# Optimization experiments

Measured on AMD Instinct MI355X. Metric: run time of the kernel, lower is better.

## Reference

```python
import jax, jax.numpy as jnp
import numpy as np

B, S, E, H = 4, 2048, 1024, 16
DK = E // H  # 64


def setup_inputs() -> dict:
    key = jax.random.key(0)
    ks = jax.random.split(key, 6)
    scale = 1.0 / np.sqrt(E)
    return {
        "x": jax.random.normal(ks[0], (B, S, E), dtype=jnp.float32),
        "Wq": jax.random.normal(ks[1], (E, E), dtype=jnp.float32) * scale,
        "Wk": jax.random.normal(ks[2], (E, E), dtype=jnp.float32) * scale,
        "Wv": jax.random.normal(ks[3], (E, E), dtype=jnp.float32) * scale,
        "Wo": jax.random.normal(ks[4], (E, E), dtype=jnp.float32) * scale,
        "theta": jax.random.normal(ks[5], (DK,), dtype=jnp.float32),
    }


def _heads(t):
    # [B,S,E] -> [B,H,S,DK]
    b, s, _ = t.shape
    return t.reshape(b, s, H, DK).transpose(0, 2, 1, 3)


def reference(x, Wq, Wk, Wv, Wo, theta):
    # nn.Linear (no bias): y = x @ W.T
    # quantum transform: independent single-qubit RX(x)->RX(theta)->  <Z> = cos(x+theta)
    q = jnp.cos(_heads(x @ Wq.T) + theta)  # [B,H,S,DK]
    k = jnp.cos(_heads(x @ Wk.T) + theta)
    v = jnp.cos(_heads(x @ Wv.T) + theta)
    scores = jnp.einsum("bhqd,bhkd->bhqk", q, k) / jnp.sqrt(jnp.float32(DK))
    attn = jax.nn.softmax(scores, axis=-1)  # dropout is identity in eval
    out = jnp.einsum("bhqk,bhkd->bhqd", attn, v)  # [B,H,S,DK]
    out = out.transpose(0, 2, 1, 3).reshape(x.shape[0], -1, E)
    return out @ Wo.T
```

## Files before the change

kernel.cpp:

```cpp
#include <hip/hip_runtime.h>

#define B_  4
#define S_  2048
#define E_  1024
#define H_  16
#define DK_ 64
#define M_  (B_*S_)

typedef __attribute__((ext_vector_type(8)))  short short8;
typedef __attribute__((ext_vector_type(4)))  float f32x4;
typedef __attribute__((ext_vector_type(16))) float f32x16;

#define QSCALE 0.18033688f

__device__ __forceinline__ unsigned short f2b(float f) {
    union { float f; unsigned u; } v; v.f = f;
    unsigned u = v.u;
    return (unsigned short)((u + 0x7fffu + ((u >> 16) & 1u)) >> 16);
}

__device__ __forceinline__ void gload_lds16(const unsigned short* g, unsigned short* l) {
    __builtin_amdgcn_global_load_lds((const __attribute__((address_space(1))) void*)g,
                                     (__attribute__((address_space(3))) void*)l, 16, 0, 0);
}

#define XN4 (M_*E_/4)
#define WN4 (E_*E_/4)
__global__ __launch_bounds__(256) void cvt_all(
    const float* __restrict__ x,
    const float* __restrict__ w0, const float* __restrict__ w1,
    const float* __restrict__ w2, const float* __restrict__ w3,
    unsigned short* __restrict__ xb, unsigned short* __restrict__ wb,
    unsigned short* __restrict__ wob) {
    int i = blockIdx.x * 256 + threadIdx.x;
    const float* src;
    unsigned short* dst;
    int idx;
    if (i < XN4) { src = x; dst = xb; idx = i; }
    else {
        int j = i - XN4;
        int z = j >> 18;
        idx = j & (WN4 - 1);
        src = (z == 0) ? w0 : (z == 1) ? w1 : (z == 2) ? w2 : w3;
        dst = (z < 3) ? wb + (size_t)z * E_ * E_ : wob;
    }
    float4 f = ((const float4*)src)[idx];
    ushort4 o;
    o.x = f2b(f.x); o.y = f2b(f.y); o.z = f2b(f.z); o.w = f2b(f.w);
    ((ushort4*)dst)[idx] = o;
}

__global__ __launch_bounds__(256) void gemm_qkv(
    const unsigned short* __restrict__ xb,
    const unsigned short* __restrict__ Wb,
    const float* __restrict__ theta,
    unsigned short* __restrict__ qb,
    unsigned short* __restrict__ kb,
    unsigned short* __restrict__ vtb)
{
    __shared__ unsigned short smem[128*144];
    unsigned short* As = smem;
    unsigned short* Bs = smem + 128*64;
    const int tid = threadIdx.x;
    const int w = tid >> 6, lane = tid & 63, quad = lane >> 4, col = lane & 15;
    const int wm = (w & 1) * 64, wn = (w >> 1) * 64;
    const int m0 = blockIdx.x * 128, n0 = blockIdx.y * 128, z = blockIdx.z;
    const unsigned short* Wz = Wb + (size_t)z * E_ * E_;
    const int srow = lane >> 3, schunk = (lane & 7) * 8;

    f32x4 acc[4][4] = {};
    for (int k0 = 0; k0 < E_; k0 += 64) {
        #pragma unroll
        for (int c = 0; c < 4; c++) {
            int row = w*32 + c*8 + srow;
            gload_lds16(&xb[(size_t)(m0+row)*E_ + k0 + schunk], &As[(w*32 + c*8)*64]);
            gload_lds16(&Wz[(size_t)(n0+row)*E_ + k0 + schunk], &Bs[(w*32 + c*8)*64]);
        }
        __syncthreads();
        #pragma unroll
        for (int kk = 0; kk < 64; kk += 32) {
            short8 a[4], b[4];
            #pragma unroll
            for (int i = 0; i < 4; i++)
                a[i] = *(const short8*)&As[(wm + i*16 + col)*64 + kk + quad*8];
            #pragma unroll
            for (int j = 0; j < 4; j++)
                b[j] = *(const short8*)&Bs[(wn + j*16 + col)*64 + kk + quad*8];
            #pragma unroll
            for (int i = 0; i < 4; i++)
                #pragma unroll
                for (int j = 0; j < 4; j++)
                    acc[i][j] = __builtin_amdgcn_mfma_f32_16x16x32_bf16(a[i], b[j], acc[i][j], 0, 0, 0);
        }
        __syncthreads();
    }

    const int bblk = m0 >> 11;
    const int sbase = m0 & (S_-1);

    if (z != 2) {
        const float qs = (z == 0) ? QSCALE : 1.0f;
        #pragma unroll
        for (int j = 0; j < 4; j++) {
            int nl = wn + j*16 + col;
            float th = theta[(n0 + nl) & 63];
            #pragma unroll
            for (int i = 0; i < 4; i++)
                #pragma unroll
                for (int r = 0; r < 4; r++) {
                    int ml = wm + i*16 + quad*4 + r;
                    int nls = nl ^ (((ml >> 2) & 3) << 4);
                    smem[ml*144 + nls] = f2b(__cosf(acc[i][j][r] + th) * qs);
                }
        }
        __syncthreads();
        unsigned short* dst = (z == 0) ? qb : kb;
        const int h0 = n0 >> 6;
        #pragma unroll
        for (int k = 0; k < 8; k++) {
            int idx = k*256 + tid;
            int chunk = idx & 7, seg = idx >> 3;
            int ml = seg >> 1, hh = seg & 1;
            int ch = chunk ^ (((ml >> 2) & 3) << 1);
            int4 val = *(const int4*)&smem[ml*144 + hh*64 + ch*8];
            size_t g = ((size_t)(bblk*H_ + h0 + hh)*S_ + sbase + ml)*DK_ + chunk*8;
            *(int4*)&dst[g] = val;
        }
    } else {
        #pragma unroll
        for (int j = 0; j < 4; j++) {
            int nl = wn + j*16 + col;
            float th = theta[(n0 + nl) & 63];
            #pragma unroll
            for (int i = 0; i < 4; i++)
                #pragma unroll
                for (int r = 0; r < 4; r++)
                    smem[nl*136 + wm + i*16 + quad*4 + r] = f2b(__cosf(acc[i][j][r] + th));
        }
        __syncthreads();
        int row = tid >> 1, halfm = (tid & 1) * 64;
        int n = n0 + row, h = n >> 6, d = n & 63;
        size_t base = ((size_t)(bblk*H_ + h)*DK_ + d)*S_ + sbase + halfm;
        #pragma unroll
        for (int k = 0; k < 8; k++)
            *(int4*)&vtb[base + k*8] = *(const int4*)&smem[row*136 + halfm + k*8];
    }
}

__global__ __launch_bounds__(256) void gemm_out(
    const unsigned short* __restrict__ ctx,
    const unsigned short* __restrict__ Wob,
    float* __restrict__ out)
{
    __shared__ unsigned short As[128*64];
    __shared__ unsigned short Bs[128*64];
    const int tid = threadIdx.x;
    const int w = tid >> 6, lane = tid & 63, quad = lane >> 4, col = lane & 15;
    const int wm = (w & 1) * 64, wn = (w >> 1) * 64;
    const int m0 = blockIdx.x * 128, n0 = blockIdx.y * 128;
    const int srow = lane >> 3, schunk = (lane & 7) * 8;

    f32x4 acc[4][4] = {};
    for (int k0 = 0; k0 < E_; k0 += 64) {
        #pragma unroll
        for (int c = 0; c < 4; c++) {
            int row = w*32 + c*8 + srow;
            gload_lds16(&ctx[(size_t)(m0+row)*E_ + k0 + schunk], &As[(w*32 + c*8)*64]);
            gload_lds16(&Wob[(size_t)(n0+row)*E_ + k0 + schunk], &Bs[(w*32 + c*8)*64]);
        }
        __syncthreads();
        #pragma unroll
        for (int kk = 0; kk < 64; kk += 32) {
            short8 a[4], b[4];
            #pragma unroll
            for (int i = 0; i < 4; i++)
                a[i] = *(const short8*)&As[(wm + i*16 + col)*64 + kk + quad*8];
            #pragma unroll
            for (int j = 0; j < 4; j++)
                b[j] = *(const short8*)&Bs[(wn + j*16 + col)*64 + kk + quad*8];
            #pragma unroll
            for (int i = 0; i < 4; i++)
                #pragma unroll
                for (int j = 0; j < 4; j++)
                    acc[i][j] = __builtin_amdgcn_mfma_f32_16x16x32_bf16(a[i], b[j], acc[i][j], 0, 0, 0);
        }
        __syncthreads();
    }
    #pragma unroll
    for (int j = 0; j < 4; j++) {
        int n = n0 + wn + j*16 + col;
        #pragma unroll
        for (int i = 0; i < 4; i++)
            #pragma unroll
            for (int r = 0; r < 4; r++) {
                int m = m0 + wm + i*16 + quad*4 + r;
                out[(size_t)m*E_ + n] = acc[i][j][r];
            }
    }
}

#define LPK 72

__global__ __launch_bounds__(256, 2) void flash_attn(
    const unsigned short* __restrict__ qb,
    const unsigned short* __restrict__ kb,
    const unsigned short* __restrict__ vtb,
    unsigned short* __restrict__ ctx)
{
    __shared__ unsigned short Kt[64*LPK];
    __shared__ unsigned short Vt[64*LPK];
    const int tid = threadIdx.x;
    const int w = tid >> 6, lane = tid & 63, col = lane & 31, half = lane >> 5;
    const int q0 = blockIdx.x * 256;
    const int bh = blockIdx.y;

    union U8 { unsigned u[4]; short8 s8; };

    short8 qf[2][4];
    #pragma unroll
    for (int qg = 0; qg < 2; qg++) {
        const unsigned short* qrow = qb + ((size_t)bh*S_ + q0 + w*64 + qg*32 + col)*DK_;
        #pragma unroll
        for (int c = 0; c < 4; c++)
            qf[qg][c] = *(const short8*)&qrow[c*16 + half*8];
    }

    float rsum[2] = {0.f, 0.f};
    f32x16 oacc[2][2] = {};

    for (int kt = 0; kt < S_; kt += 64) {
        __syncthreads();
        for (int i = tid; i < 512; i += 256) {
            int row = i >> 3, c8 = (i & 7) * 8;
            *(int4*)&Kt[row*LPK + c8] = *(const int4*)&kb [((size_t)bh*S_  + kt + row)*DK_ + c8];
            *(int4*)&Vt[row*LPK + c8] = *(const int4*)&vtb[((size_t)bh*DK_ + row)*S_ + kt + c8];
        }
        __syncthreads();

        #pragma unroll
        for (int t = 0; t < 2; t++) {
            short8 kf[4];
            #pragma unroll
            for (int c = 0; c < 4; c++)
                kf[c] = *(const short8*)&Kt[(t*32 + col)*LPK + c*16 + half*8];
            short8 vf[2][2];
            #pragma unroll
            for (int kc = 0; kc < 2; kc++)
                #pragma unroll
                for (int dt = 0; dt < 2; dt++)
                    vf[kc][dt] = *(const short8*)&Vt[(dt*32 + col)*LPK + t*32 + kc*16 + half*8];

            #pragma unroll
            for (int qg = 0; qg < 2; qg++) {
                f32x16 sacc = {};
                #pragma unroll
                for (int c = 0; c < 4; c++)
                    sacc = __builtin_amdgcn_mfma_f32_32x32x16_bf16(kf[c], qf[qg][c], sacc, 0, 0, 0);
                unsigned pk[4][2];
                #pragma unroll
                for (int rg = 0; rg < 4; rg++) {
                    float p0 = __builtin_amdgcn_exp2f(sacc[rg*4+0]);
                    float p1 = __builtin_amdgcn_exp2f(sacc[rg*4+1]);
                    float p2 = __builtin_amdgcn_exp2f(sacc[rg*4+2]);
                    float p3 = __builtin_amdgcn_exp2f(sacc[rg*4+3]);
                    rsum[qg] += (p0 + p1) + (p2 + p3);
                    pk[rg][0] = __builtin_amdgcn_perm(__float_as_uint(p1), __float_as_uint(p0), 0x07060302u);
                    pk[rg][1] = __builtin_amdgcn_perm(__float_as_uint(p3), __float_as_uint(p2), 0x07060302u);
                }
                #pragma unroll
                for (int kc = 0; kc < 2; kc++) {
                    const int lo = 2*kc, hi = 2*kc + 1;
                    unsigned t0 = half ? pk[lo][0] : pk[hi][0];
                    unsigned t1 = half ? pk[lo][1] : pk[hi][1];
                    unsigned r0 = __shfl_xor((int)t0, 32);
                    unsigned r1 = __shfl_xor((int)t1, 32);
                    U8 pa;
                    pa.u[0] = half ? r0 : pk[lo][0];
                    pa.u[1] = half ? r1 : pk[lo][1];
                    pa.u[2] = half ? pk[hi][0] : r0;
                    pa.u[3] = half ? pk[hi][1] : r1;
                    #pragma unroll
                    for (int dt = 0; dt < 2; dt++)
                        oacc[qg][dt] = __builtin_amdgcn_mfma_f32_32x32x16_bf16(pa.s8, vf[kc][dt], oacc[qg][dt], 0, 0, 0);
                }
            }
        }
    }

    const int b = bh >> 4, h = bh & 15;
    #pragma unroll
    for (int qg = 0; qg < 2; qg++) {
        float l = rsum[qg] + __shfl_xor(rsum[qg], 32);
        float inv = 1.0f / l;
        #pragma unroll
        for (int rg = 0; rg < 4; rg++)
            #pragma unroll
            for (int rr = 0; rr < 4; rr++) {
                int row = rr + rg*8 + half*4;
                float invr = __shfl(inv, row);
                int s = q0 + w*64 + qg*32 + row;
                size_t rowoff = ((size_t)(b*S_ + s))*E_ + h*64;
                #pragma unroll
                for (int dt = 0; dt < 2; dt++)
                    ctx[rowoff + dt*32 + col] = f2b(oacc[qg][dt][rg*4 + rr] * invr);
            }
    }
}

extern "C" void kernel_launch(void* const* d_in, const int* in_sizes, int n_in,
                              void* d_out, int out_size, void* d_ws, size_t ws_size,
                              hipStream_t stream) {
    (void)in_sizes; (void)n_in; (void)out_size; (void)ws_size;
    const float* x     = (const float*)d_in[0];
    const float* Wq    = (const float*)d_in[1];
    const float* Wk    = (const float*)d_in[2];
    const float* Wv    = (const float*)d_in[3];
    const float* Wo    = (const float*)d_in[4];
    const float* theta = (const float*)d_in[5];
    float* out = (float*)d_out;

    unsigned short* ws  = (unsigned short*)d_ws;
    unsigned short* xb  = ws;
    unsigned short* Wb  = xb  + (size_t)M_*E_;
    unsigned short* Wob = Wb  + (size_t)3*E_*E_;
    unsigned short* qb  = Wob + (size_t)E_*E_;
    unsigned short* kb  = qb  + (size_t)B_*H_*S_*DK_;
    unsigned short* vtb = kb  + (size_t)B_*H_*S_*DK_;
    unsigned short* ctx = xb;

    cvt_all<<<(XN4 + 4*WN4)/256, 256, 0, stream>>>(x, Wq, Wk, Wv, Wo, xb, Wb, Wob);

    gemm_qkv<<<dim3(M_/128, E_/128, 3), 256, 0, stream>>>(xb, Wb, theta, qb, kb, vtb);
    flash_attn<<<dim3(S_/256, B_*H_), 256, 0, stream>>>(qb, kb, vtb, ctx);
    gemm_out<<<dim3(M_/128, E_/128), 256, 0, stream>>>(ctx, Wob, out);
}
```

Measured before the change: 298.7 us.

## Shrink attention query tile, flip MFMA operands for direct vector epilogue stores

Flash attention now handles 32 query rows per wave instead of 64, doubling the grid and raising launch bounds to 4 blocks per CU for better occupancy. The cost is K/V tiles being reloaded from LDS and global memory twice as often. The GEMM main loop is factored into a template that can swap MFMA operands, so each lane holds contiguous output columns. The QKV and output-projection epilogues then write ushort4 or float4 directly, dropping the LDS staging transpose and its barrier, with less coalesced global stores as the trade-off.

```diff
diff --git a/kernel.cpp b/kernel.cpp
--- a/kernel.cpp
+++ b/kernel.cpp
@@ -50,6 +50,44 @@
     ((ushort4*)dst)[idx] = o;
 }
 
+template<bool FLIP>
+__device__ __forceinline__ void gemm_kloop(
+    const unsigned short* __restrict__ Ag, const unsigned short* __restrict__ Bg,
+    unsigned short* As, unsigned short* Bs,
+    int m0, int n0, int w, int lane, f32x4 acc[4][4])
+{
+    const int quad = lane >> 4, col = lane & 15;
+    const int wm = (w & 1) * 64, wn = (w >> 1) * 64;
+    const int srow = lane >> 3, schunk = (lane & 7) * 8;
+    for (int k0 = 0; k0 < E_; k0 += 64) {
+        #pragma unroll
+        for (int c = 0; c < 4; c++) {
+            int row = w*32 + c*8 + srow;
+            gload_lds16(&Ag[(size_t)(m0+row)*E_ + k0 + schunk], &As[(w*32 + c*8)*64]);
+            gload_lds16(&Bg[(size_t)(n0+row)*E_ + k0 + schunk], &Bs[(w*32 + c*8)*64]);
+        }
+        __syncthreads();
+        #pragma unroll
+        for (int kk = 0; kk < 64; kk += 32) {
+            short8 a[4], b[4];
+            #pragma unroll
+            for (int i = 0; i < 4; i++)
+                a[i] = *(const short8*)&As[(wm + i*16 + col)*64 + kk + quad*8];
+            #pragma unroll
+            for (int j = 0; j < 4; j++)
+                b[j] = *(const short8*)&Bs[(wn + j*16 + col)*64 + kk + quad*8];
+            #pragma unroll
+            for (int i = 0; i < 4; i++)
+                #pragma unroll
+                for (int j = 0; j < 4; j++)
+                    acc[i][j] = FLIP
+                      ? __builtin_amdgcn_mfma_f32_16x16x32_bf16(b[j], a[i], acc[i][j], 0, 0, 0)
+                      : __builtin_amdgcn_mfma_f32_16x16x32_bf16(a[i], b[j], acc[i][j], 0, 0, 0);
+        }
+        __syncthreads();
+    }
+}
+
 __global__ __launch_bounds__(256) void gemm_qkv(
     const unsigned short* __restrict__ xb,
     const unsigned short* __restrict__ Wb,
@@ -58,92 +96,54 @@
     unsigned short* __restrict__ kb,
     unsigned short* __restrict__ vtb)
 {
-    __shared__ unsigned short smem[128*144];
-    unsigned short* As = smem;
-    unsigned short* Bs = smem + 128*64;
+    __shared__ unsigned short As[128*64];
+    __shared__ unsigned short Bs[128*64];
     const int tid = threadIdx.x;
     const int w = tid >> 6, lane = tid & 63, quad = lane >> 4, col = lane & 15;
     const int wm = (w & 1) * 64, wn = (w >> 1) * 64;
     const int m0 = blockIdx.x * 128, n0 = blockIdx.y * 128, z = blockIdx.z;
     const unsigned short* Wz = Wb + (size_t)z * E_ * E_;
-    const int srow = lane >> 3, schunk = (lane & 7) * 8;
+    const int bblk = m0 >> 11, sbase = m0 & (S_-1);
 
     f32x4 acc[4][4] = {};
-    for (int k0 = 0; k0 < E_; k0 += 64) {
-        #pragma unroll
-        for (int c = 0; c < 4; c++) {
-            int row = w*32 + c*8 + srow;
-            gload_lds16(&xb[(size_t)(m0+row)*E_ + k0 + schunk], &As[(w*32 + c*8)*64]);
-            gload_lds16(&Wz[(size_t)(n0+row)*E_ + k0 + schunk], &Bs[(w*32 + c*8)*64]);
-        }
-        __syncthreads();
-        #pragma unroll
-        for (int kk = 0; kk < 64; kk += 32) {
-            short8 a[4], b[4];
-            #pragma unroll
-            for (int i = 0; i < 4; i++)
-                a[i] = *(const short8*)&As[(wm + i*16 + col)*64 + kk + quad*8];
-            #pragma unroll
-            for (int j = 0; j < 4; j++)
-                b[j] = *(const short8*)&Bs[(wn + j*16 + col)*64 + kk + quad*8];
-            #pragma unroll
-            for (int i = 0; i < 4; i++)
-                #pragma unroll
-                for (int j = 0; j < 4; j++)
-                    acc[i][j] = __builtin_amdgcn_mfma_f32_16x16x32_bf16(a[i], b[j], acc[i][j], 0, 0, 0);
-        }
-        __syncthreads();
-    }
-
-    const int bblk = m0 >> 11;
-    const int sbase = m0 & (S_-1);
-
     if (z != 2) {
+        gemm_kloop<true>(xb, Wz, As, Bs, m0, n0, w, lane, acc);
         const float qs = (z == 0) ? QSCALE : 1.0f;
+        unsigned short* dst = (z == 0) ? qb : kb;
         #pragma unroll
         for (int j = 0; j < 4; j++) {
-            int nl = wn + j*16 + col;
-            float th = theta[(n0 + nl) & 63];
-            #pragma unroll
-            for (int i = 0; i < 4; i++)
-                #pragma unroll
-                for (int r = 0; r < 4; r++) {
-                    int ml = wm + i*16 + quad*4 + r;
-                    int nls = nl ^ (((ml >> 2) & 3) << 4);
-                    smem[ml*144 + nls] = f2b(__cosf(acc[i][j][r] + th) * qs);
-                }
-        }
-        __syncthreads();
-        unsigned short* dst = (z == 0) ? qb : kb;
-        const int h0 = n0 >> 6;
-        #pragma unroll
-        for (int k = 0; k < 8; k++) {
-            int idx = k*256 + tid;
-            int chunk = idx & 7, seg = idx >> 3;
-            int ml = seg >> 1, hh = seg & 1;
-            int ch = chunk ^ (((ml >> 2) & 3) << 1);
-            int4 val = *(const int4*)&smem[ml*144 + hh*64 + ch*8];
-            size_t g = ((size_t)(bblk*H_ + h0 + hh)*S_ + sbase + ml)*DK_ + chunk*8;
-            *(int4*)&dst[g] = val;
+            int nb = wn + j*16 + quad*4;
+            int h = (n0 + nb) >> 6, d0 = nb & 63;
+            float4 th = *(const float4*)&theta[d0];
+            #pragma unroll
+            for (int i = 0; i < 4; i++) {
+                int s = sbase + wm + i*16 + col;
+                ushort4 o;
+                o.x = f2b(__cosf(acc[i][j][0] + th.x) * qs);
+                o.y = f2b(__cosf(acc[i][j][1] + th.y) * qs);
+                o.z = f2b(__cosf(acc[i][j][2] + th.z) * qs);
+                o.w = f2b(__cosf(acc[i][j][3] + th.w) * qs);
+                *(ushort4*)&dst[((size_t)(bblk*H_ + h)*S_ + s)*DK_ + d0] = o;
+            }
         }
     } else {
+        gemm_kloop<false>(xb, Wz, As, Bs, m0, n0, w, lane, acc);
         #pragma unroll
         for (int j = 0; j < 4; j++) {
-            int nl = wn + j*16 + col;
-            float th = theta[(n0 + nl) & 63];
-            #pragma unroll
-            for (int i = 0; i < 4; i++)
-                #pragma unroll
-                for (int r = 0; r < 4; r++)
-                    smem[nl*136 + wm + i*16 + quad*4 + r] = f2b(__cosf(acc[i][j][r] + th));
-        }
-        __syncthreads();
-        int row = tid >> 1, halfm = (tid & 1) * 64;
-        int n = n0 + row, h = n >> 6, d = n & 63;
-        size_t base = ((size_t)(bblk*H_ + h)*DK_ + d)*S_ + sbase + halfm;
-        #pragma unroll
-        for (int k = 0; k < 8; k++)
-            *(int4*)&vtb[base + k*8] = *(const int4*)&smem[row*136 + halfm + k*8];
+            int n = n0 + wn + j*16 + col;
+            int h = n >> 6, d = n & 63;
+            float th = theta[d];
+            #pragma unroll
+            for (int i = 0; i < 4; i++) {
+                int s0 = sbase + wm + i*16 + quad*4;
+                ushort4 o;
+                o.x = f2b(__cosf(acc[i][j][0] + th));
+                o.y = f2b(__cosf(acc[i][j][1] + th));
+                o.z = f2b(__cosf(acc[i][j][2] + th));
+                o.w = f2b(__cosf(acc[i][j][3] + th));
+                *(ushort4*)&vtb[((size_t)(bblk*H_ + h)*DK_ + d)*S_ + s0] = o;
+            }
+        }
     }
 }
 
@@ -158,50 +158,23 @@
     const int w = tid >> 6, lane = tid & 63, quad = lane >> 4, col = lane & 15;
     const int wm = (w & 1) * 64, wn = (w >> 1) * 64;
     const int m0 = blockIdx.x * 128, n0 = blockIdx.y * 128;
-    const int srow = lane >> 3, schunk = (lane & 7) * 8;
 
     f32x4 acc[4][4] = {};
-    for (int k0 = 0; k0 < E_; k0 += 64) {
-        #pragma unroll
-        for (int c = 0; c < 4; c++) {
-            int row = w*32 + c*8 + srow;
-            gload_lds16(&ctx[(size_t)(m0+row)*E_ + k0 + schunk], &As[(w*32 + c*8)*64]);
-            gload_lds16(&Wob[(size_t)(n0+row)*E_ + k0 + schunk], &Bs[(w*32 + c*8)*64]);
-        }
-        __syncthreads();
-        #pragma unroll
-        for (int kk = 0; kk < 64; kk += 32) {
-            short8 a[4], b[4];
-            #pragma unroll
-            for (int i = 0; i < 4; i++)
-                a[i] = *(const short8*)&As[(wm + i*16 + col)*64 + kk + quad*8];
-            #pragma unroll
-            for (int j = 0; j < 4; j++)
-                b[j] = *(const short8*)&Bs[(wn + j*16 + col)*64 + kk + quad*8];
-            #pragma unroll
-            for (int i = 0; i < 4; i++)
-                #pragma unroll
-                for (int j = 0; j < 4; j++)
-                    acc[i][j] = __builtin_amdgcn_mfma_f32_16x16x32_bf16(a[i], b[j], acc[i][j], 0, 0, 0);
-        }
-        __syncthreads();
-    }
+    gemm_kloop<true>(ctx, Wob, As, Bs, m0, n0, w, lane, acc);
     #pragma unroll
     for (int j = 0; j < 4; j++) {
-        int n = n0 + wn + j*16 + col;
-        #pragma unroll
-        for (int i = 0; i < 4; i++)
-            #pragma unroll
-            for (int r = 0; r < 4; r++) {
-                int m = m0 + wm + i*16 + quad*4 + r;
-                out[(size_t)m*E_ + n] = acc[i][j][r];
-            }
+        int nb = n0 + wn + j*16 + quad*4;
+        #pragma unroll
+        for (int i = 0; i < 4; i++) {
+            int m = m0 + wm + i*16 + col;
+            *(f32x4*)&out[(size_t)m*E_ + nb] = acc[i][j];
+        }
     }
 }
 
 #define LPK 72
 
-__global__ __launch_bounds__(256, 2) void flash_attn(
+__global__ __launch_bounds__(256, 4) void flash_attn(
     const unsigned short* __restrict__ qb,
     const unsigned short* __restrict__ kb,
     const unsigned short* __restrict__ vtb,
@@ -211,22 +184,21 @@
     __shared__ unsigned short Vt[64*LPK];
     const int tid = threadIdx.x;
     const int w = tid >> 6, lane = tid & 63, col = lane & 31, half = lane >> 5;
-    const int q0 = blockIdx.x * 256;
+    const int q0 = blockIdx.x * 128;
     const int bh = blockIdx.y;
 
     union U8 { unsigned u[4]; short8 s8; };
 
-    short8 qf[2][4];
-    #pragma unroll
-    for (int qg = 0; qg < 2; qg++) {
-        const unsigned short* qrow = qb + ((size_t)bh*S_ + q0 + w*64 + qg*32 + col)*DK_;
+    short8 qf[4];
+    {
+        const unsigned short* qrow = qb + ((size_t)bh*S_ + q0 + w*32 + col)*DK_;
         #pragma unroll
         for (int c = 0; c < 4; c++)
-            qf[qg][c] = *(const short8*)&qrow[c*16 + half*8];
-    }
-
-    float rsum[2] = {0.f, 0.f};
-    f32x16 oacc[2][2] = {};
+            qf[c] = *(const short8*)&qrow[c*16 + half*8];
+    }
+
+    float rsum = 0.f;
+    f32x16 oacc[2] = {};
 
     for (int kt = 0; kt < S_; kt += 64) {
         __syncthreads();
@@ -239,72 +211,59 @@
 
         #pragma unroll
         for (int t = 0; t < 2; t++) {
-            short8 kf[4];
-            #pragma unroll
-            for (int c = 0; c < 4; c++)
-                kf[c] = *(const short8*)&Kt[(t*32 + col)*LPK + c*16 + half*8];
-            short8 vf[2][2];
-            #pragma unroll
-            for (int kc = 0; kc < 2; kc++)
+            f32x16 sacc = {};
+            #pragma unroll
+            for (int c = 0; c < 4; c++) {
+                short8 kf = *(const short8*)&Kt[(t*32 + col)*LPK + c*16 + half*8];
+                sacc = __builtin_amdgcn_mfma_f32_32x32x16_bf16(kf, qf[c], sacc, 0, 0, 0);
+            }
+            unsigned pk[4][2];
+            #pragma unroll
+            for (int rg = 0; rg < 4; rg++) {
+                float p0 = __builtin_amdgcn_exp2f(sacc[rg*4+0]);
+                float p1 = __builtin_amdgcn_exp2f(sacc[rg*4+1]);
+                float p2 = __builtin_amdgcn_exp2f(sacc[rg*4+2]);
+                float p3 = __builtin_amdgcn_exp2f(sacc[rg*4+3]);
+                rsum += (p0 + p1) + (p2 + p3);
+                pk[rg][0] = __builtin_amdgcn_perm(__float_as_uint(p1), __float_as_uint(p0), 0x07060302u);
+                pk[rg][1] = __builtin_amdgcn_perm(__float_as_uint(p3), __float_as_uint(p2), 0x07060302u);
+            }
+            #pragma unroll
+            for (int kc = 0; kc < 2; kc++) {
+                const int lo = 2*kc, hi = 2*kc + 1;
+                unsigned t0 = half ? pk[lo][0] : pk[hi][0];
+                unsigned t1 = half ? pk[lo][1] : pk[hi][1];
+                unsigned r0 = __shfl_xor((int)t0, 32);
+                unsigned r1 = __shfl_xor((int)t1, 32);
+                U8 pa;
+                pa.u[0] = half ? r0 : pk[lo][0];
+                pa.u[1] = half ? r1 : pk[lo][1];
+                pa.u[2] = half ? pk[hi][0] : r0;
+                pa.u[3] = half ? pk[hi][1] : r1;
                 #pragma unroll
-                for (int dt = 0; dt < 2; dt++)
-                    vf[kc][dt] = *(const short8*)&Vt[(dt*32 + col)*LPK + t*32 + kc*16 + half*8];
-
-            #pragma unroll
-            for (int qg = 0; qg < 2; qg++) {
-                f32x16 sacc = {};
-                #pragma unroll
-                for (int c = 0; c < 4; c++)
-                    sacc = __builtin_amdgcn_mfma_f32_32x32x16_bf16(kf[c], qf[qg][c], sacc, 0, 0, 0);
-                unsigned pk[4][2];
-                #pragma unroll
-                for (int rg = 0; rg < 4; rg++) {
-                    float p0 = __builtin_amdgcn_exp2f(sacc[rg*4+0]);
-                    float p1 = __builtin_amdgcn_exp2f(sacc[rg*4+1]);
-                    float p2 = __builtin_amdgcn_exp2f(sacc[rg*4+2]);
-                    float p3 = __builtin_amdgcn_exp2f(sacc[rg*4+3]);
-                    rsum[qg] += (p0 + p1) + (p2 + p3);
-                    pk[rg][0] = __builtin_amdgcn_perm(__float_as_uint(p1), __float_as_uint(p0), 0x07060302u);
-                    pk[rg][1] = __builtin_amdgcn_perm(__float_as_uint(p3), __float_as_uint(p2), 0x07060302u);
+                for (int dt = 0; dt < 2; dt++) {
+                    short8 vf = *(const short8*)&Vt[(dt*32 + col)*LPK + t*32 + kc*16 + half*8];
+                    oacc[dt] = __builtin_amdgcn_mfma_f32_32x32x16_bf16(pa.s8, vf, oacc[dt], 0, 0, 0);
                 }
-                #pragma unroll
-                for (int kc = 0; kc < 2; kc++) {
-                    const int lo = 2*kc, hi = 2*kc + 1;
-                    unsigned t0 = half ? pk[lo][0] : pk[hi][0];
-                    unsigned t1 = half ? pk[lo][1] : pk[hi][1];
-                    unsigned r0 = __shfl_xor((int)t0, 32);
-                    unsigned r1 = __shfl_xor((int)t1, 32);
-                    U8 pa;
-                    pa.u[0] = half ? r0 : pk[lo][0];
-                    pa.u[1] = half ? r1 : pk[lo][1];
-                    pa.u[2] = half ? pk[hi][0] : r0;
-                    pa.u[3] = half ? pk[hi][1] : r1;
-                    #pragma unroll
-                    for (int dt = 0; dt < 2; dt++)
-                        oacc[qg][dt] = __builtin_amdgcn_mfma_f32_32x32x16_bf16(pa.s8, vf[kc][dt], oacc[qg][dt], 0, 0, 0);
-                }
             }
         }
     }
 
     const int b = bh >> 4, h = bh & 15;
+    float l = rsum + __shfl_xor(rsum, 32);
+    float inv = 1.0f / l;
     #pragma unroll
-    for (int qg = 0; qg < 2; qg++) {
-        float l = rsum[qg] + __shfl_xor(rsum[qg], 32);
-        float inv = 1.0f / l;
-        #pragma unroll
-        for (int rg = 0; rg < 4; rg++)
-            #pragma unroll
-            for (int rr = 0; rr < 4; rr++) {
-                int row = rr + rg*8 + half*4;
-                float invr = __shfl(inv, row);
-                int s = q0 + w*64 + qg*32 + row;
-                size_t rowoff = ((size_t)(b*S_ + s))*E_ + h*64;
-                #pragma unroll
-                for (int dt = 0; dt < 2; dt++)
-                    ctx[rowoff + dt*32 + col] = f2b(oacc[qg][dt][rg*4 + rr] * invr);
-            }
-    }
+    for (int rg = 0; rg < 4; rg++)
+        #pragma unroll
+        for (int rr = 0; rr < 4; rr++) {
+            int row = rr + rg*8 + half*4;
+            float invr = __shfl(inv, row);
+            int s = q0 + w*32 + row;
+            size_t rowoff = ((size_t)(b*S_ + s))*E_ + h*64;
+            #pragma unroll
+            for (int dt = 0; dt < 2; dt++)
+                ctx[rowoff + dt*32 + col] = f2b(oacc[dt][rg*4 + rr] * invr);
+        }
 }
 
 extern "C" void kernel_launch(void* const* d_in, const int* in_sizes, int n_in,
@@ -331,6 +290,6 @@
     cvt_all<<<(XN4 + 4*WN4)/256, 256, 0, stream>>>(x, Wq, Wk, Wv, Wo, xb, Wb, Wob);
 
     gemm_qkv<<<dim3(M_/128, E_/128, 3), 256, 0, stream>>>(xb, Wb, theta, qb, kb, vtb);
-    flash_attn<<<dim3(S_/256, B_*H_), 256, 0, stream>>>(qb, kb, vtb, ctx);
+    flash_attn<<<dim3(S_/128, B_*H_), 256, 0, stream>>>(qb, kb, vtb, ctx);
     gemm_out<<<dim3(M_/128, E_/128), 256, 0, stream>>>(ctx, Wob, out);
 }
```

New measurement: 307.2 us. 1.03x slower.
